# Optimization experiments

Measured on AMD Instinct MI355X. Metric: run time of the kernel, lower is better.

Reference implementation:

```python
import math
import jax, jax.numpy as jnp
import numpy as np

B, S, D = 4, 2048, 1024
EPS_LN = 1e-5
EPS_MAS = 1e-9


def layernorm(x, g, b):
    m = jnp.mean(x, axis=-1, keepdims=True)
    v = jnp.mean(jnp.square(x - m), axis=-1, keepdims=True)
    return (x - m) * jax.lax.rsqrt(v + EPS_LN) * g + b


def spl(x, proto_w, mu_w, mu_b, gate):
    # match_values = x @ proto^T / sqrt(d);  comp = silu(x @ mu^T + b)
    match = jnp.einsum('bsd,od->bso', x, proto_w) / math.sqrt(x.shape[-1])
    comp = jax.nn.silu(jnp.einsum('bsd,od->bso', x, mu_w) + mu_b)
    return comp, match, gate


def branch(comp, match, gate, passthrough):
    # mas_normalize on the 1-D gate vector (cost), broadcast over [B,S,D]
    cost = gate / (jnp.max(jnp.abs(gate)) + EPS_MAS)
    rl = match - cost
    mrl = jax.nn.relu(rl)
    mask = (rl > 0).astype(comp.dtype)
    return comp * mrl + passthrough * (1.0 - mask)


def causal_attention(q, k, v):
    # num_heads = 1, head_dim = D, is_causal=True
    scale = 1.0 / math.sqrt(q.shape[-1])
    scores = jnp.einsum('bqd,bkd->bqk', q, k) * scale
    causal = jnp.tril(jnp.ones((q.shape[1], k.shape[1]), dtype=bool))
    scores = jnp.where(causal, scores, jnp.asarray(-1e9, scores.dtype))
    p = jax.nn.softmax(scores, axis=-1)
    return jnp.einsum('bqk,bkd->bqd', p, v)


def setup_inputs() -> dict:
    key = jax.random.key(0)
    ks = jax.random.split(key, 16)
    d = D
    std = 0.02
    inp = {
        'x': jax.random.normal(ks[0], (B, S, d), jnp.float32),
        'ln_g': jnp.ones((d,), jnp.float32),
        'ln_b': jnp.zeros((d,), jnp.float32),
    }
    names = ['q', 'k', 'v', 'o']
    for i, n in enumerate(names):
        inp[f'{n}_mu_w'] = std * jax.random.normal(ks[1 + 3 * i], (d, d), jnp.float32)
        inp[f'{n}_mu_b'] = jnp.zeros((d,), jnp.float32)
        inp[f'{n}_proto'] = std * jax.random.normal(ks[2 + 3 * i], (d, d), jnp.float32)
        inp[f'{n}_gate'] = 0.1 * jax.random.normal(ks[3 + 3 * i], (d,), jnp.float32)
    return inp


def reference(x, ln_g, ln_b,
              q_mu_w, q_mu_b, q_proto, q_gate,
              k_mu_w, k_mu_b, k_proto, k_gate,
              v_mu_w, v_mu_b, v_proto, v_gate,
              o_mu_w, o_mu_b, o_proto, o_gate):
    ln1_out = layernorm(x, ln_g, ln_b)

    c_q, mv_q, g_q = spl(ln1_out, q_proto, q_mu_w, q_mu_b, q_gate)
    c_k, mv_k, g_k = spl(ln1_out, k_proto, k_mu_w, k_mu_b, k_gate)
    c_v, mv_v, g_v = spl(ln1_out, v_proto, v_mu_w, v_mu_b, v_gate)

    q = branch(c_q, mv_q, g_q, ln1_out)
    k = branch(c_k, mv_k, g_k, ln1_out)
    v = branch(c_v, mv_v, g_v, ln1_out)

    attn_out = causal_attention(q, k, v)

    c_o, mv_o, g_o = spl(attn_out, o_proto, o_mu_w, o_mu_b, o_gate)
    masked_o = branch(c_o, mv_o, g_o, attn_out)

    x_out = x + masked_o
    return x_out
```

## Files before the change

kernel.cpp:

```cpp
#include <hip/hip_runtime.h>
#include <hip/hip_bf16.h>
#include <cmath>
#include <cstdint>

typedef _Float16 f16;
typedef _Float16 f16x8 __attribute__((ext_vector_type(8)));
typedef float f32x4 __attribute__((ext_vector_type(4)));

#define D_ 1024
#define S_ 2048


__device__ __forceinline__ void gload_lds16(const void* g, void* l) {
  __builtin_amdgcn_global_load_lds(
      (const __attribute__((address_space(1))) void*)(unsigned long long)(uintptr_t)g,
      (__attribute__((address_space(3))) void*)(unsigned int)(uintptr_t)l,
      16, 0, 0);
}

__device__ __forceinline__ int lds_off(int row, int cb) {
  return (row << 5) + ((cb ^ ((row >> 1) & 3)) << 3);
}

__device__ __forceinline__ void split1024(float v, f16& h, f16& l) {
  float s = v * 1024.f;
  h = (f16)s;
  l = (f16)(s - (float)h);
}

__device__ __forceinline__ void stage_tile(const f16* __restrict__ src, int ld,
                                           f16* lds, int wid, int lane) {
  const int r = (wid << 5) + (lane >> 2);
  const int c = (lane & 3) ^ ((r >> 1) & 3);
  const f16* g0 = src + (size_t)r * ld + (c << 3);
  gload_lds16(g0, lds + (wid << 10));
  gload_lds16(g0 + (size_t)(ld << 4), lds + (wid << 10) + 512);
}

__global__ __launch_bounds__(256) void convert_w(
    const float* __restrict__ s0, const float* __restrict__ s1,
    const float* __restrict__ s2, const float* __restrict__ s3,
    const float* __restrict__ s4, const float* __restrict__ s5,
    const float* __restrict__ s6, const float* __restrict__ s7,
    f16* __restrict__ dst) {
  const float* srcs[8] = {s0, s1, s2, s3, s4, s5, s6, s7};
  const float* sp = srcs[blockIdx.y];
  f16* hi = dst + (size_t)blockIdx.y * 2097152;
  f16* lo = hi + 1048576;
  const int i = (blockIdx.x * 256 + threadIdx.x) << 2;
  float4 f = *(const float4*)(sp + i);
  __align__(8) f16 h4[4], l4[4];
  split1024(f.x, h4[0], l4[0]); split1024(f.y, h4[1], l4[1]);
  split1024(f.z, h4[2], l4[2]); split1024(f.w, h4[3], l4[3]);
  *(uint2*)(hi + i) = *(uint2*)h4;
  *(uint2*)(lo + i) = *(uint2*)l4;
}

__global__ __launch_bounds__(256) void cost_k(
    const float* __restrict__ g0, const float* __restrict__ g1,
    const float* __restrict__ g2, const float* __restrict__ g3,
    float* __restrict__ cost) {
  const float* gp = blockIdx.x == 0 ? g0 : blockIdx.x == 1 ? g1
                   : blockIdx.x == 2 ? g2 : g3;
  const int t = threadIdx.x;
  float4 v = *(const float4*)(gp + (t << 2));
  float mx = fmaxf(fmaxf(fabsf(v.x), fabsf(v.y)), fmaxf(fabsf(v.z), fabsf(v.w)));
  for (int o = 32; o; o >>= 1) mx = fmaxf(mx, __shfl_xor(mx, o, 64));
  __shared__ float red[4];
  if ((t & 63) == 0) red[t >> 6] = mx;
  __syncthreads();
  mx = fmaxf(fmaxf(red[0], red[1]), fmaxf(red[2], red[3]));
  const float den = mx + 1e-9f;
  float4 o = {v.x / den, v.y / den, v.z / den, v.w / den};
  *(float4*)(cost + (blockIdx.x << 10) + (t << 2)) = o;
}

__global__ __launch_bounds__(256) void layernorm_k(
    const float* __restrict__ x, const float* __restrict__ g,
    const float* __restrict__ bta, f16* __restrict__ Lh, f16* __restrict__ Ll) {
  const int row = blockIdx.x, t = threadIdx.x;
  const float* xr = x + (size_t)row * D_;
  float4 v = *(const float4*)(xr + (t << 2));
  float s = v.x + v.y + v.z + v.w;
  float q = v.x * v.x + v.y * v.y + v.z * v.z + v.w * v.w;
  for (int o = 32; o; o >>= 1) { s += __shfl_xor(s, o, 64); q += __shfl_xor(q, o, 64); }
  __shared__ float red[8];
  const int wid = t >> 6;
  if ((t & 63) == 0) { red[wid] = s; red[4 + wid] = q; }
  __syncthreads();
  s = red[0] + red[1] + red[2] + red[3];
  q = red[4] + red[5] + red[6] + red[7];
  const float mean = s * (1.f / D_);
  const float var = q * (1.f / D_) - mean * mean;
  const float inv = 1.f / sqrtf(var + 1e-5f);
  float4 gv = *(const float4*)(g + (t << 2));
  float4 bv = *(const float4*)(bta + (t << 2));
  __align__(8) f16 h4[4], l4[4];
  split1024((v.x - mean) * inv * gv.x + bv.x, h4[0], l4[0]);
  split1024((v.y - mean) * inv * gv.y + bv.y, h4[1], l4[1]);
  split1024((v.z - mean) * inv * gv.z + bv.z, h4[2], l4[2]);
  split1024((v.w - mean) * inv * gv.w + bv.w, h4[3], l4[3]);
  const size_t off = (size_t)row * D_ + (t << 2);
  *(uint2*)(Lh + off) = *(uint2*)h4;
  *(uint2*)(Ll + off) = *(uint2*)l4;
}

#define MFMA16(a, b, c) __builtin_amdgcn_mfma_f32_16x16x32_f16((a), (b), (c), 0, 0, 0)

template <int EPI, int MUP>
__global__ __launch_bounds__(1024) void dual_gemm_v5(
    const f16* __restrict__ Ah, const f16* __restrict__ Al,
    const f16* __restrict__ Wph, const f16* __restrict__ Wpl,
    const f16* __restrict__ Wmh, const f16* __restrict__ Wml,
    const float* __restrict__ bias, const float* __restrict__ cost,
    const f16* __restrict__ passh, const f16* __restrict__ passl,
    const float* __restrict__ xres, f16* __restrict__ outh,
    f16* __restrict__ outl, float* __restrict__ outf) {
  __shared__ __align__(16) f16 smem[65536];
  const int tid = threadIdx.x, wid = tid >> 6, lane = tid & 63;
  const int row0 = blockIdx.x << 8, col0 = blockIdx.y << 7;
  const int wr = (wid & 3) << 6;
  const int wc = (wid >> 2) << 5;
  const int arow = lane & 15, cbk = lane >> 4;

  const int srow = tid >> 2;
  const int scA = ((tid & 3) ^ ((srow >> 1) & 3)) << 3;
  const int wrow = srow & 127;
  const int scW = ((tid & 3) ^ ((wrow >> 1) & 3)) << 3;
  const int wsel = tid >> 9;
  const int dstA = wid << 9;
  const int dstW = 16384 + (wid << 9);
  const int dstW2 = 24576 + (wid << 9);

  const f16* pAh = Ah + (size_t)(row0 + srow) * D_ + scA;
  const f16* pAl = Al + (size_t)(row0 + srow) * D_ + scA;
  const f16* pW1 = (wsel ? Wpl : Wph) + (size_t)(col0 + wrow) * D_ + scW;
  const f16* pW2 = (wsel ? Wml : Wmh) + (size_t)(col0 + wrow) * D_ + scW;

  const f32x4 zero = {0.f, 0.f, 0.f, 0.f};
  f32x4 accP[4][2], accM[4][2];
#pragma unroll
  for (int m = 0; m < 4; ++m)
#pragma unroll
    for (int n = 0; n < 2; ++n) { accP[m][n] = zero; accM[m][n] = zero; }

  int aoff[4], boff[2];
#pragma unroll
  for (int m = 0; m < 4; ++m) aoff[m] = lds_off(wr + m * 16 + arow, cbk);
#pragma unroll
  for (int n = 0; n < 2; ++n) boff[n] = lds_off(wc + n * 16 + arow, cbk);

  gload_lds16(pAh, smem + dstA);
  gload_lds16(pAl, smem + 8192 + dstA);
  gload_lds16(pW1, smem + dstW);
  gload_lds16(pW2, smem + dstW2);

  int cur = 0;
  for (int t = 0; t < 32; ++t) {
    const f16* bb = smem + (cur << 15);
    f16* nb = smem + ((cur ^ 1) << 15);
    const int kn = (t < 31) ? ((t + 1) << 5) : 0;

    gload_lds16(pAh + kn, nb + dstA);
    gload_lds16(pAl + kn, nb + 8192 + dstA);
    gload_lds16(pW1 + kn, nb + dstW);
    gload_lds16(pW2 + kn, nb + dstW2);
    asm volatile("s_waitcnt vmcnt(4)\n\ts_barrier" ::: "memory");
    __builtin_amdgcn_sched_barrier(0);

    f16x8 ah[4], al[4];
#pragma unroll
    for (int m = 0; m < 4; ++m) {
      ah[m] = *(const f16x8*)&bb[aoff[m]];
      al[m] = *(const f16x8*)&bb[8192 + aoff[m]];
    }
    __builtin_amdgcn_s_setprio(1);
#pragma unroll
    for (int n = 0; n < 2; ++n) {
      const f16x8 bph = *(const f16x8*)&bb[16384 + boff[n]];
      const f16x8 bpl = *(const f16x8*)&bb[20480 + boff[n]];
      const f16x8 bmh = *(const f16x8*)&bb[24576 + boff[n]];
      const f16x8 bml = *(const f16x8*)&bb[28672 + boff[n]];
#pragma unroll
      for (int m = 0; m < 4; ++m) {
        accP[m][n] = MFMA16(ah[m], bph, accP[m][n]);
        accP[m][n] = MFMA16(ah[m], bpl, accP[m][n]);
        accP[m][n] = MFMA16(al[m], bph, accP[m][n]);
        accM[m][n] = MFMA16(ah[m], bmh, accM[m][n]);
        accM[m][n] = MFMA16(ah[m], bml, accM[m][n]);
        if (MUP == 3) accM[m][n] = MFMA16(al[m], bmh, accM[m][n]);
      }
    }
    __builtin_amdgcn_s_setprio(0);
    asm volatile("s_waitcnt lgkmcnt(0)\n\ts_barrier" ::: "memory");
    cur ^= 1;
  }

#pragma unroll
  for (int m = 0; m < 4; ++m) {
    const int rb = row0 + wr + m * 16 + ((lane >> 4) << 2);
#pragma unroll
    for (int n = 0; n < 2; ++n) {
      const int col = col0 + wc + n * 16 + (lane & 15);
      const float cb2 = cost[col], bbv = bias[col];
#pragma unroll
      for (int j = 0; j < 4; ++j) {
        const size_t off = (size_t)(rb + j) * D_ + col;
        const float match = accP[m][n][j] * (1.f / 33554432.f);
        const float pre = accM[m][n][j] * (1.f / 1048576.f) + bbv;
        const float comp = pre / (1.f + expf(-pre));
        const float rl = match - cb2;
        float ov;
        if (rl > 0.f) ov = comp * rl;
        else ov = ((float)passh[off] + (float)passl[off]) * (1.f / 1024.f);
        if (EPI == 0) {
          f16 h, l; split1024(ov, h, l);
          outh[off] = h; outl[off] = l;
        } else {
          outf[off] = xres[off] + ov;
        }
      }
    }
  }
}

__global__ __launch_bounds__(256) void transpose_v(
    const f16* __restrict__ Vh, const f16* __restrict__ Vl,
    f16* __restrict__ VTh, f16* __restrict__ VTl) {
  const int iz = blockIdx.z, b = iz & 3;
  const f16* src = (iz >> 2) ? Vl : Vh;
  f16* dst = (iz >> 2) ? VTl : VTh;
  const int d0 = blockIdx.x << 6, s0 = blockIdx.y << 6;
  __shared__ f16 tl[64][65];
  const int c = threadIdx.x & 63, r4 = threadIdx.x >> 6;
  const f16* vb = src + (size_t)b * S_ * D_;
#pragma unroll
  for (int i = 0; i < 16; ++i) {
    const int sr = (r4 << 4) + i;
    tl[sr][c] = vb[(size_t)(s0 + sr) * D_ + d0 + c];
  }
  __syncthreads();
  f16* db = dst + (size_t)b * D_ * S_;
#pragma unroll
  for (int i = 0; i < 16; ++i) {
    const int dr = (r4 << 4) + i;
    db[(size_t)(d0 + dr) * S_ + s0 + c] = tl[c][dr];
  }
}

__global__ __launch_bounds__(256, 2) void scores_gemm(
    const f16* __restrict__ Qh, const f16* __restrict__ Ql,
    const f16* __restrict__ Kh, const f16* __restrict__ Kl,
    float* __restrict__ SC) {
  const int rt = blockIdx.x, ct = blockIdx.y, b = blockIdx.z;
  if (ct > rt) return;
  __shared__ __align__(16) f16 lQh[4096], lQl[4096], lKh[4096], lKl[4096];
  const int tid = threadIdx.x, wid = tid >> 6, lane = tid & 63;
  const int row0 = rt << 7, col0 = ct << 7;
  const int wr = (wid >> 1) << 6, wc = (wid & 1) << 6;
  const int arow = lane & 15, cb = lane >> 4;
  const f32x4 zero = {0.f, 0.f, 0.f, 0.f};
  f32x4 acc[4][4];
#pragma unroll
  for (int m = 0; m < 4; ++m)
#pragma unroll
    for (int n = 0; n < 4; ++n) acc[m][n] = zero;
  const f16* Qhb = Qh + ((size_t)b * S_ + row0) * D_;
  const f16* Qlb = Ql + ((size_t)b * S_ + row0) * D_;
  const f16* Khb = Kh + ((size_t)b * S_ + col0) * D_;
  const f16* Klb = Kl + ((size_t)b * S_ + col0) * D_;
  for (int k = 0; k < D_; k += 32) {
    stage_tile(Qhb + k, D_, lQh, wid, lane);
    stage_tile(Qlb + k, D_, lQl, wid, lane);
    stage_tile(Khb + k, D_, lKh, wid, lane);
    stage_tile(Klb + k, D_, lKl, wid, lane);
    __syncthreads();
    f16x8 bh[4], bl[4];
#pragma unroll
    for (int n = 0; n < 4; ++n) {
      const int bo = lds_off(wc + n * 16 + arow, cb);
      bh[n] = *(const f16x8*)&lKh[bo];
      bl[n] = *(const f16x8*)&lKl[bo];
    }
#pragma unroll
    for (int m = 0; m < 4; ++m) {
      const int ao = lds_off(wr + m * 16 + arow, cb);
      f16x8 ah = *(const f16x8*)&lQh[ao];
      f16x8 al = *(const f16x8*)&lQl[ao];
#pragma unroll
      for (int n = 0; n < 4; ++n) {
        acc[m][n] = __builtin_amdgcn_mfma_f32_16x16x32_f16(ah, bh[n], acc[m][n], 0, 0, 0);
        acc[m][n] = __builtin_amdgcn_mfma_f32_16x16x32_f16(ah, bl[n], acc[m][n], 0, 0, 0);
        acc[m][n] = __builtin_amdgcn_mfma_f32_16x16x32_f16(al, bh[n], acc[m][n], 0, 0, 0);
      }
    }
    __syncthreads();
  }
  float* scb = SC + (size_t)b * S_ * S_;
#pragma unroll
  for (int m = 0; m < 4; ++m) {
    const int rb = row0 + wr + m * 16 + ((lane >> 4) << 2);
#pragma unroll
    for (int n = 0; n < 4; ++n) {
      const int col = col0 + wc + n * 16 + (lane & 15);
#pragma unroll
      for (int j = 0; j < 4; ++j)
        scb[(size_t)(rb + j) * S_ + col] = acc[m][n][j] * (1.f / 33554432.f);
    }
  }
}

__global__ __launch_bounds__(256) void softmax_rows(float* __restrict__ SC) {
  const int r = blockIdx.x;
  const int s = r & 2047;
  float* rowf = SC + (size_t)r * S_;
  const int t = threadIdx.x, c0 = t << 3;
  float f[8];
  float4 u0 = *(const float4*)(rowf + c0);
  float4 u1 = *(const float4*)(rowf + c0 + 4);
  f[0] = u0.x; f[1] = u0.y; f[2] = u0.z; f[3] = u0.w;
  f[4] = u1.x; f[5] = u1.y; f[6] = u1.z; f[7] = u1.w;
  float mx = -3.0e38f;
#pragma unroll
  for (int j = 0; j < 8; ++j)
    if (c0 + j <= s) mx = fmaxf(mx, f[j]);
  for (int o = 32; o; o >>= 1) mx = fmaxf(mx, __shfl_xor(mx, o, 64));
  __shared__ float red[8];
  const int wid = t >> 6;
  if ((t & 63) == 0) red[wid] = mx;
  __syncthreads();
  mx = fmaxf(fmaxf(red[0], red[1]), fmaxf(red[2], red[3]));
  float e[8];
  float sum = 0.f;
#pragma unroll
  for (int j = 0; j < 8; ++j) {
    e[j] = (c0 + j <= s) ? expf(f[j] - mx) : 0.f;
    sum += e[j];
  }
  for (int o = 32; o; o >>= 1) sum += __shfl_xor(sum, o, 64);
  if ((t & 63) == 0) red[4 + wid] = sum;
  __syncthreads();
  sum = red[4] + red[5] + red[6] + red[7];
  f16* rowh = (f16*)rowf;
  __align__(16) f16 ph[8], pl[8];
#pragma unroll
  for (int j = 0; j < 8; ++j) {
    float p = (e[j] / sum) * 2048.f;
    ph[j] = (f16)p;
    pl[j] = (f16)(p - (float)ph[j]);
  }
  *(uint4*)(rowh + c0) = *(uint4*)ph;
  *(uint4*)(rowh + 2048 + c0) = *(uint4*)pl;
}

__global__ __launch_bounds__(256, 2) void pv_gemm(
    const f16* __restrict__ P, const f16* __restrict__ VTh,
    const f16* __restrict__ VTl, f16* __restrict__ Ath, f16* __restrict__ Atl) {
  const int rt = blockIdx.x, ct = blockIdx.y, b = blockIdx.z;
  __shared__ __align__(16) f16 lPh[4096], lPl[4096], lVh[4096], lVl[4096];
  const int tid = threadIdx.x, wid = tid >> 6, lane = tid & 63;
  const int row0 = rt << 7, col0 = ct << 7;
  const int wr = (wid >> 1) << 6, wc = (wid & 1) << 6;
  const int arow = lane & 15, cb = lane >> 4;
  const f32x4 zero = {0.f, 0.f, 0.f, 0.f};
  f32x4 acc[4][4];
#pragma unroll
  for (int m = 0; m < 4; ++m)
#pragma unroll
    for (int n = 0; n < 4; ++n) acc[m][n] = zero;
  const f16* Pb = P + ((size_t)b * S_ + row0) * 4096;
  const f16* Vhb = VTh + (size_t)b * D_ * S_ + (size_t)col0 * S_;
  const f16* Vlb = VTl + (size_t)b * D_ * S_ + (size_t)col0 * S_;
  const int kend = (rt + 1) << 7;
  for (int k = 0; k < kend; k += 32) {
    stage_tile(Pb + k, 4096, lPh, wid, lane);
    stage_tile(Pb + 2048 + k, 4096, lPl, wid, lane);
    stage_tile(Vhb + k, S_, lVh, wid, lane);
    stage_tile(Vlb + k, S_, lVl, wid, lane);
    __syncthreads();
    f16x8 bh[4], bl[4];
#pragma unroll
    for (int n = 0; n < 4; ++n) {
      const int bo = lds_off(wc + n * 16 + arow, cb);
      bh[n] = *(const f16x8*)&lVh[bo];
      bl[n] = *(const f16x8*)&lVl[bo];
    }
#pragma unroll
    for (int m = 0; m < 4; ++m) {
      const int ao = lds_off(wr + m * 16 + arow, cb);
      f16x8 ah = *(const f16x8*)&lPh[ao];
      f16x8 al = *(const f16x8*)&lPl[ao];
#pragma unroll
      for (int n = 0; n < 4; ++n) {
        acc[m][n] = __builtin_amdgcn_mfma_f32_16x16x32_f16(ah, bh[n], acc[m][n], 0, 0, 0);
        acc[m][n] = __builtin_amdgcn_mfma_f32_16x16x32_f16(ah, bl[n], acc[m][n], 0, 0, 0);
        acc[m][n] = __builtin_amdgcn_mfma_f32_16x16x32_f16(al, bh[n], acc[m][n], 0, 0, 0);
      }
    }
    __syncthreads();
  }
#pragma unroll
  for (int m = 0; m < 4; ++m) {
    const int rb = row0 + wr + m * 16 + ((lane >> 4) << 2);
#pragma unroll
    for (int n = 0; n < 4; ++n) {
      const int col = col0 + wc + n * 16 + (lane & 15);
#pragma unroll
      for (int j = 0; j < 4; ++j) {
        const float at = acc[m][n][j] * (1.f / 2097152.f);
        const size_t off = ((size_t)b * S_ + rb + j) * D_ + col;
        f16 h, l; split1024(at, h, l);
        Ath[off] = h; Atl[off] = l;
      }
    }
  }
}

extern "C" void kernel_launch(void* const* d_in, const int* in_sizes, int n_in,
                              void* d_out, int out_size, void* d_ws, size_t ws_size,
                              hipStream_t stream) {
  (void)in_sizes; (void)n_in; (void)out_size; (void)ws_size;
  const float* x      = (const float*)d_in[0];
  const float* ln_g   = (const float*)d_in[1];
  const float* ln_b   = (const float*)d_in[2];
  const float* q_mu_w = (const float*)d_in[3];
  const float* q_mu_b = (const float*)d_in[4];
  const float* q_pro  = (const float*)d_in[5];
  const float* q_gate = (const float*)d_in[6];
  const float* k_mu_w = (const float*)d_in[7];
  const float* k_mu_b = (const float*)d_in[8];
  const float* k_pro  = (const float*)d_in[9];
  const float* k_gate = (const float*)d_in[10];
  const float* v_mu_w = (const float*)d_in[11];
  const float* v_mu_b = (const float*)d_in[12];
  const float* v_pro  = (const float*)d_in[13];
  const float* v_gate = (const float*)d_in[14];
  const float* o_mu_w = (const float*)d_in[15];
  const float* o_mu_b = (const float*)d_in[16];
  const float* o_pro  = (const float*)d_in[17];
  const float* o_gate = (const float*)d_in[18];

  char* w = (char*)d_ws;
  f16* WB = (f16*)w;
  const size_t WS = 2097152;
  f16* Lh  = (f16*)(w + 33554432);
  f16* Ll  = (f16*)(w + 50331648);
  f16* Qh  = (f16*)(w + 67108864);
  f16* Ql  = (f16*)(w + 83886080);
  f16* Kh  = (f16*)(w + 100663296);
  f16* Kl  = (f16*)(w + 117440512);
  f16* VTh = (f16*)(w + 134217728);
  f16* VTl = (f16*)(w + 150994944);
  float* SC = (float*)(w + 167772160);
  float* COST = (float*)(w + 234881024);
  f16* Vh = (f16*)SC;
  f16* Vl = (f16*)(w + 184549376);
  f16* Ath = Qh;  f16* Atl = Ql;

  convert_w<<<dim3(1024, 8), 256, 0, stream>>>(
      q_pro, q_mu_w, k_pro, k_mu_w, v_pro, v_mu_w, o_pro, o_mu_w, WB);
  cost_k<<<4, 256, 0, stream>>>(q_gate, k_gate, v_gate, o_gate, COST);
  layernorm_k<<<8192, 256, 0, stream>>>(x, ln_g, ln_b, Lh, Ll);

  dual_gemm_v5<0, 3><<<dim3(32, 8), 1024, 0, stream>>>(
      Lh, Ll, WB, WB + 1048576, WB + WS, WB + WS + 1048576,
      q_mu_b, COST, Lh, Ll, nullptr, Qh, Ql, nullptr);
  dual_gemm_v5<0, 3><<<dim3(32, 8), 1024, 0, stream>>>(
      Lh, Ll, WB + 2 * WS, WB + 2 * WS + 1048576, WB + 3 * WS, WB + 3 * WS + 1048576,
      k_mu_b, COST + 1024, Lh, Ll, nullptr, Kh, Kl, nullptr);
  dual_gemm_v5<0, 3><<<dim3(32, 8), 1024, 0, stream>>>(
      Lh, Ll, WB + 4 * WS, WB + 4 * WS + 1048576, WB + 5 * WS, WB + 5 * WS + 1048576,
      v_mu_b, COST + 2048, Lh, Ll, nullptr, Vh, Vl, nullptr);

  transpose_v<<<dim3(16, 32, 8), 256, 0, stream>>>(Vh, Vl, VTh, VTl);
  scores_gemm<<<dim3(16, 16, 4), 256, 0, stream>>>(Qh, Ql, Kh, Kl, SC);
  softmax_rows<<<8192, 256, 0, stream>>>(SC);
  pv_gemm<<<dim3(16, 8, 4), 256, 0, stream>>>((const f16*)SC, VTh, VTl, Ath, Atl);

  dual_gemm_v5<1, 2><<<dim3(32, 8), 1024, 0, stream>>>(
      Ath, Atl, WB + 6 * WS, WB + 6 * WS + 1048576, WB + 7 * WS, WB + 7 * WS + 1048576,
      o_mu_b, COST + 3072, Ath, Atl, x, nullptr, nullptr, (float*)d_out);
}
```

Before: 690.9 us.

## Double-buffer LDS staging in scores and PV GEMMs with 8 waves per block

Rewrites the attention scores and P·V GEMM kernels so that global→LDS loads for the next K-slice are issued while MFMAs run on the current buffer. Synchronisation uses explicit vmcnt and lgkmcnt waits with barriers, and MFMA sections are wrapped in raised wave priority. Blocks grow from 256 to 512 threads, so each wave covers a 64x32 sub-tile instead of 64x64. This is meant to hide load latency and raise the number of waves per CU. The trade-off is doubled LDS per block, which may cap occupancy, plus extra redundant A-fragment reads per wave.

```diff
diff --git a/kernel.cpp b/kernel.cpp
--- a/kernel.cpp
+++ b/kernel.cpp
@@ -28,14 +28,7 @@
   l = (f16)(s - (float)h);
 }
 
-__device__ __forceinline__ void stage_tile(const f16* __restrict__ src, int ld,
-                                           f16* lds, int wid, int lane) {
-  const int r = (wid << 5) + (lane >> 2);
-  const int c = (lane & 3) ^ ((r >> 1) & 3);
-  const f16* g0 = src + (size_t)r * ld + (c << 3);
-  gload_lds16(g0, lds + (wid << 10));
-  gload_lds16(g0 + (size_t)(ld << 4), lds + (wid << 10) + 512);
-}
+#define MFMA16(a, b, c) __builtin_amdgcn_mfma_f32_16x16x32_f16((a), (b), (c), 0, 0, 0)
 
 __global__ __launch_bounds__(256) void convert_w(
     const float* __restrict__ s0, const float* __restrict__ s1,
@@ -105,8 +98,6 @@
   *(uint2*)(Ll + off) = *(uint2*)l4;
 }
 
-#define MFMA16(a, b, c) __builtin_amdgcn_mfma_f32_16x16x32_f16((a), (b), (c), 0, 0, 0)
-
 template <int EPI, int MUP>
 __global__ __launch_bounds__(1024) void dual_gemm_v5(
     const f16* __restrict__ Ah, const f16* __restrict__ Al,
@@ -248,60 +239,88 @@
   }
 }
 
-__global__ __launch_bounds__(256, 2) void scores_gemm(
+__global__ __launch_bounds__(512) void scores_v5(
     const f16* __restrict__ Qh, const f16* __restrict__ Ql,
     const f16* __restrict__ Kh, const f16* __restrict__ Kl,
     float* __restrict__ SC) {
   const int rt = blockIdx.x, ct = blockIdx.y, b = blockIdx.z;
   if (ct > rt) return;
-  __shared__ __align__(16) f16 lQh[4096], lQl[4096], lKh[4096], lKl[4096];
+  __shared__ __align__(16) f16 smem[32768];
   const int tid = threadIdx.x, wid = tid >> 6, lane = tid & 63;
   const int row0 = rt << 7, col0 = ct << 7;
-  const int wr = (wid >> 1) << 6, wc = (wid & 1) << 6;
-  const int arow = lane & 15, cb = lane >> 4;
+  const int wr = (wid & 1) << 6;
+  const int wc = (wid >> 1) << 5;
+  const int arow = lane & 15, cbk = lane >> 4;
+
+  const int srow = tid >> 2;
+  const int sc4 = ((tid & 3) ^ ((srow >> 1) & 3)) << 3;
+  const int dstb = wid << 9;
+
+  const f16* pQh = Qh + ((size_t)b * S_ + row0 + srow) * D_ + sc4;
+  const f16* pQl = Ql + ((size_t)b * S_ + row0 + srow) * D_ + sc4;
+  const f16* pKh = Kh + ((size_t)b * S_ + col0 + srow) * D_ + sc4;
+  const f16* pKl = Kl + ((size_t)b * S_ + col0 + srow) * D_ + sc4;
+
   const f32x4 zero = {0.f, 0.f, 0.f, 0.f};
-  f32x4 acc[4][4];
+  f32x4 acc[4][2];
 #pragma unroll
   for (int m = 0; m < 4; ++m)
 #pragma unroll
-    for (int n = 0; n < 4; ++n) acc[m][n] = zero;
-  const f16* Qhb = Qh + ((size_t)b * S_ + row0) * D_;
-  const f16* Qlb = Ql + ((size_t)b * S_ + row0) * D_;
-  const f16* Khb = Kh + ((size_t)b * S_ + col0) * D_;
-  const f16* Klb = Kl + ((size_t)b * S_ + col0) * D_;
-  for (int k = 0; k < D_; k += 32) {
-    stage_tile(Qhb + k, D_, lQh, wid, lane);
-    stage_tile(Qlb + k, D_, lQl, wid, lane);
-    stage_tile(Khb + k, D_, lKh, wid, lane);
-    stage_tile(Klb + k, D_, lKl, wid, lane);
-    __syncthreads();
-    f16x8 bh[4], bl[4];
-#pragma unroll
-    for (int n = 0; n < 4; ++n) {
-      const int bo = lds_off(wc + n * 16 + arow, cb);
-      bh[n] = *(const f16x8*)&lKh[bo];
-      bl[n] = *(const f16x8*)&lKl[bo];
-    }
+    for (int n = 0; n < 2; ++n) acc[m][n] = zero;
+
+  int aoff[4], boff[2];
+#pragma unroll
+  for (int m = 0; m < 4; ++m) aoff[m] = lds_off(wr + m * 16 + arow, cbk);
+#pragma unroll
+  for (int n = 0; n < 2; ++n) boff[n] = lds_off(wc + n * 16 + arow, cbk);
+
+  gload_lds16(pQh, smem + dstb);
+  gload_lds16(pQl, smem + 4096 + dstb);
+  gload_lds16(pKh, smem + 8192 + dstb);
+  gload_lds16(pKl, smem + 12288 + dstb);
+
+  int cur = 0;
+  for (int t = 0; t < 32; ++t) {
+    const f16* bb = smem + (cur << 14);
+    f16* nb = smem + ((cur ^ 1) << 14);
+    const int kn = (t < 31) ? ((t + 1) << 5) : 0;
+
+    gload_lds16(pQh + kn, nb + dstb);
+    gload_lds16(pQl + kn, nb + 4096 + dstb);
+    gload_lds16(pKh + kn, nb + 8192 + dstb);
+    gload_lds16(pKl + kn, nb + 12288 + dstb);
+    asm volatile("s_waitcnt vmcnt(4)\n\ts_barrier" ::: "memory");
+    __builtin_amdgcn_sched_barrier(0);
+
+    f16x8 ah[4], al[4];
 #pragma unroll
     for (int m = 0; m < 4; ++m) {
-      const int ao = lds_off(wr + m * 16 + arow, cb);
-      f16x8 ah = *(const f16x8*)&lQh[ao];
-      f16x8 al = *(const f16x8*)&lQl[ao];
-#pragma unroll
-      for (int n = 0; n < 4; ++n) {
-        acc[m][n] = __builtin_amdgcn_mfma_f32_16x16x32_f16(ah, bh[n], acc[m][n], 0, 0, 0);
-        acc[m][n] = __builtin_amdgcn_mfma_f32_16x16x32_f16(ah, bl[n], acc[m][n], 0, 0, 0);
-        acc[m][n] = __builtin_amdgcn_mfma_f32_16x16x32_f16(al, bh[n], acc[m][n], 0, 0, 0);
+      ah[m] = *(const f16x8*)&bb[aoff[m]];
+      al[m] = *(const f16x8*)&bb[4096 + aoff[m]];
+    }
+    __builtin_amdgcn_s_setprio(1);
+#pragma unroll
+    for (int n = 0; n < 2; ++n) {
+      const f16x8 bh = *(const f16x8*)&bb[8192 + boff[n]];
+      const f16x8 bl = *(const f16x8*)&bb[12288 + boff[n]];
+#pragma unroll
+      for (int m = 0; m < 4; ++m) {
+        acc[m][n] = MFMA16(ah[m], bh, acc[m][n]);
+        acc[m][n] = MFMA16(ah[m], bl, acc[m][n]);
+        acc[m][n] = MFMA16(al[m], bh, acc[m][n]);
       }
     }
-    __syncthreads();
-  }
+    __builtin_amdgcn_s_setprio(0);
+    asm volatile("s_waitcnt lgkmcnt(0)\n\ts_barrier" ::: "memory");
+    cur ^= 1;
+  }
+
   float* scb = SC + (size_t)b * S_ * S_;
 #pragma unroll
   for (int m = 0; m < 4; ++m) {
     const int rb = row0 + wr + m * 16 + ((lane >> 4) << 2);
 #pragma unroll
-    for (int n = 0; n < 4; ++n) {
+    for (int n = 0; n < 2; ++n) {
       const int col = col0 + wc + n * 16 + (lane & 15);
 #pragma unroll
       for (int j = 0; j < 4; ++j)
@@ -353,57 +372,87 @@
   *(uint4*)(rowh + 2048 + c0) = *(uint4*)pl;
 }
 
-__global__ __launch_bounds__(256, 2) void pv_gemm(
+__global__ __launch_bounds__(512) void pv_v5(
     const f16* __restrict__ P, const f16* __restrict__ VTh,
     const f16* __restrict__ VTl, f16* __restrict__ Ath, f16* __restrict__ Atl) {
   const int rt = blockIdx.x, ct = blockIdx.y, b = blockIdx.z;
-  __shared__ __align__(16) f16 lPh[4096], lPl[4096], lVh[4096], lVl[4096];
+  __shared__ __align__(16) f16 smem[32768];
   const int tid = threadIdx.x, wid = tid >> 6, lane = tid & 63;
   const int row0 = rt << 7, col0 = ct << 7;
-  const int wr = (wid >> 1) << 6, wc = (wid & 1) << 6;
-  const int arow = lane & 15, cb = lane >> 4;
+  const int wr = (wid & 1) << 6;
+  const int wc = (wid >> 1) << 5;
+  const int arow = lane & 15, cbk = lane >> 4;
+
+  const int srow = tid >> 2;
+  const int sc4 = ((tid & 3) ^ ((srow >> 1) & 3)) << 3;
+  const int dstb = wid << 9;
+
+  const f16* pPh = P + ((size_t)b * S_ + row0 + srow) * 4096 + sc4;
+  const f16* pPl = pPh + 2048;
+  const f16* pVh = VTh + (size_t)b * D_ * S_ + (size_t)(col0 + srow) * S_ + sc4;
+  const f16* pVl = VTl + (size_t)b * D_ * S_ + (size_t)(col0 + srow) * S_ + sc4;
+
   const f32x4 zero = {0.f, 0.f, 0.f, 0.f};
-  f32x4 acc[4][4];
+  f32x4 acc[4][2];
 #pragma unroll
   for (int m = 0; m < 4; ++m)
 #pragma unroll
-    for (int n = 0; n < 4; ++n) acc[m][n] = zero;
-  const f16* Pb = P + ((size_t)b * S_ + row0) * 4096;
-  const f16* Vhb = VTh + (size_t)b * D_ * S_ + (size_t)col0 * S_;
-  const f16* Vlb = VTl + (size_t)b * D_ * S_ + (size_t)col0 * S_;
-  const int kend = (rt + 1) << 7;
-  for (int k = 0; k < kend; k += 32) {
-    stage_tile(Pb + k, 4096, lPh, wid, lane);
-    stage_tile(Pb + 2048 + k, 4096, lPl, wid, lane);
-    stage_tile(Vhb + k, S_, lVh, wid, lane);
-    stage_tile(Vlb + k, S_, lVl, wid, lane);
-    __syncthreads();
-    f16x8 bh[4], bl[4];
-#pragma unroll
-    for (int n = 0; n < 4; ++n) {
-      const int bo = lds_off(wc + n * 16 + arow, cb);
-      bh[n] = *(const f16x8*)&lVh[bo];
-      bl[n] = *(const f16x8*)&lVl[bo];
-    }
+    for (int n = 0; n < 2; ++n) acc[m][n] = zero;
+
+  int aoff[4], boff[2];
+#pragma unroll
+  for (int m = 0; m < 4; ++m) aoff[m] = lds_off(wr + m * 16 + arow, cbk);
+#pragma unroll
+  for (int n = 0; n < 2; ++n) boff[n] = lds_off(wc + n * 16 + arow, cbk);
+
+  const int steps = (rt + 1) << 2;
+
+  gload_lds16(pPh, smem + dstb);
+  gload_lds16(pPl, smem + 4096 + dstb);
+  gload_lds16(pVh, smem + 8192 + dstb);
+  gload_lds16(pVl, smem + 12288 + dstb);
+
+  int cur = 0;
+  for (int t = 0; t < steps; ++t) {
+    const f16* bb = smem + (cur << 14);
+    f16* nb = smem + ((cur ^ 1) << 14);
+    const int kn = (t < steps - 1) ? ((t + 1) << 5) : 0;
+
+    gload_lds16(pPh + kn, nb + dstb);
+    gload_lds16(pPl + kn, nb + 4096 + dstb);
+    gload_lds16(pVh + kn, nb + 8192 + dstb);
+    gload_lds16(pVl + kn, nb + 12288 + dstb);
+    asm volatile("s_waitcnt vmcnt(4)\n\ts_barrier" ::: "memory");
+    __builtin_amdgcn_sched_barrier(0);
+
+    f16x8 ah[4], al[4];
 #pragma unroll
     for (int m = 0; m < 4; ++m) {
-      const int ao = lds_off(wr + m * 16 + arow, cb);
-      f16x8 ah = *(const f16x8*)&lPh[ao];
-      f16x8 al = *(const f16x8*)&lPl[ao];
-#pragma unroll
-      for (int n = 0; n < 4; ++n) {
-        acc[m][n] = __builtin_amdgcn_mfma_f32_16x16x32_f16(ah, bh[n], acc[m][n], 0, 0, 0);
-        acc[m][n] = __builtin_amdgcn_mfma_f32_16x16x32_f16(ah, bl[n], acc[m][n], 0, 0, 0);
-        acc[m][n] = __builtin_amdgcn_mfma_f32_16x16x32_f16(al, bh[n], acc[m][n], 0, 0, 0);
+      ah[m] = *(const f16x8*)&bb[aoff[m]];
+      al[m] = *(const f16x8*)&bb[4096 + aoff[m]];
+    }
+    __builtin_amdgcn_s_setprio(1);
+#pragma unroll
+    for (int n = 0; n < 2; ++n) {
+      const f16x8 bh = *(const f16x8*)&bb[8192 + boff[n]];
+      const f16x8 bl = *(const f16x8*)&bb[12288 + boff[n]];
+#pragma unroll
+      for (int m = 0; m < 4; ++m) {
+        acc[m][n] = MFMA16(ah[m], bh, acc[m][n]);
+        acc[m][n] = MFMA16(ah[m], bl, acc[m][n]);
+        acc[m][n] = MFMA16(al[m], bh, acc[m][n]);
       }
     }
-    __syncthreads();
-  }
+    __builtin_amdgcn_s_setprio(0);
+    asm volatile("s_waitcnt lgkmcnt(0)\n\ts_barrier" ::: "memory");
+    cur ^= 1;
+  }
+
 #pragma unroll
   for (int m = 0; m < 4; ++m) {
     const int rb = row0 + wr + m * 16 + ((lane >> 4) << 2);
 #pragma unroll
-    for (int n = 0; n < 4; ++n) {
+    for (int n = 0; n < 2; ++n) {
       const int col = col0 + wc + n * 16 + (lane & 15);
 #pragma unroll
       for (int j = 0; j < 4; ++j) {
@@ -473,9 +522,9 @@
       v_mu_b, COST + 2048, Lh, Ll, nullptr, Vh, Vl, nullptr);
 
   transpose_v<<<dim3(16, 32, 8), 256, 0, stream>>>(Vh, Vl, VTh, VTl);
-  scores_gemm<<<dim3(16, 16, 4), 256, 0, stream>>>(Qh, Ql, Kh, Kl, SC);
+  scores_v5<<<dim3(16, 16, 4), 512, 0, stream>>>(Qh, Ql, Kh, Kl, SC);
   softmax_rows<<<8192, 256, 0, stream>>>(SC);
-  pv_gemm<<<dim3(16, 8, 4), 256, 0, stream>>>((const f16*)SC, VTh, VTl, Ath, Atl);
+  pv_v5<<<dim3(16, 8, 4), 512, 0, stream>>>((const f16*)SC, VTh, VTl, Ath, Atl);
 
   dual_gemm_v5<1, 2><<<dim3(32, 8), 1024, 0, stream>>>(
       Ath, Atl, WB + 6 * WS, WB + 6 * WS + 1048576, WB + 7 * WS, WB + 7 * WS + 1048576,
```

Measured after the change: 696.5 us. Within noise of the previous version (+0.8%).
